# Performance work log

Measured on AMD Instinct MI355X. Metric: run time of the kernel, lower is better.

Reference implementation:

```python
import jax, jax.numpy as jnp
import numpy as np

# |V| = 1,048,576 -> depth = bit_length(|V|-1) = 20, perfect binary tree
DEPTH = 20
N_DIMS = 128
SIZE = (1 << (DEPTH + 1)) - 1  # 2,097,151 tree nodes, each a Linear(n_dims,1) weight row


def setup_inputs() -> dict:
    key = jax.random.key(0)
    # all nn.Linear(n_dims, 1, bias=False) weights stacked into one [SIZE, N_DIMS] table
    W = jax.random.normal(key, (SIZE, N_DIMS), dtype=jnp.float32) * 0.02
    return {"W": W, "v_j_idx": 12345, "u_k_idx": 777777}


def _root_to_leaf_path(u_k_idx):
    # tree index of the leaf is u_k + 2^depth - 1; path node at level l of the
    # perfect tree is ((leaf_idx + 1) >> (depth - l)) - 1, for l = 0..depth.
    t = jnp.asarray(u_k_idx, dtype=jnp.int32) + (1 << DEPTH)  # tgt_idx + 1
    levels = jnp.arange(DEPTH + 1, dtype=jnp.int32)
    return jnp.right_shift(t, DEPTH - levels) - 1  # [depth+1], root -> leaf


def reference(W, v_j_idx, u_k_idx):
    leaf_off = (1 << DEPTH) - 1
    # x = nodes[v_leaf].weight.clone().data  (detached copy of the leaf's weight row)
    x = jax.lax.stop_gradient(W[v_j_idx + leaf_off])  # [n_dims]
    path = _root_to_leaf_path(u_k_idx)                # [depth+1]
    logits = W[path] @ x                              # [depth+1] tiny gather + dot
    prob_of_collocation = jnp.prod(jax.nn.sigmoid(logits))
    return prob_of_collocation.reshape(1, 1)          # matches torch [1,1] output
```

## Files before the change

### kernel.cpp

```cpp
#include <hip/hip_runtime.h>
#include <hip/hip_bf16.h>

#define BT_DEPTH 20
#define BT_NDIMS 128

__global__ __launch_bounds__(256) void BinaryTree_18734647345500_kernel(
    const float* __restrict__ W,
    const int* __restrict__ v_j_idx,
    const int* __restrict__ u_k_idx,
    float* __restrict__ out)
{
    __shared__ float xs[BT_NDIMS];
    __shared__ float logits[BT_DEPTH + 1];

    const int tid  = threadIdx.x;
    const int wave = tid >> 6;
    const int lane = tid & 63;

    const int v = v_j_idx[0];
    const int u = u_k_idx[0];

    const long long leaf = (long long)v + ((1 << BT_DEPTH) - 1);
    if (tid < BT_NDIMS) {
        xs[tid] = W[leaf * BT_NDIMS + tid];
    }
    __syncthreads();

    const unsigned t = (unsigned)u + (1u << BT_DEPTH);

    for (int l = wave; l <= BT_DEPTH; l += 4) {
        const long long node = (long long)(t >> (BT_DEPTH - l)) - 1;
        const float* __restrict__ row = W + node * (long long)BT_NDIMS;

        const float2 rv = *(const float2*)(row + lane * 2);
        const float2 xv = *(const float2*)(&xs[lane * 2]);
        float s = rv.x * xv.x + rv.y * xv.y;

        s += __shfl_xor(s, 32, 64);
        s += __shfl_xor(s, 16, 64);
        s += __shfl_xor(s,  8, 64);
        s += __shfl_xor(s,  4, 64);
        s += __shfl_xor(s,  2, 64);
        s += __shfl_xor(s,  1, 64);

        if (lane == 0) logits[l] = s;
    }
    __syncthreads();

    if (tid == 0) {
        float p = 1.0f;
        #pragma unroll
        for (int l = 0; l <= BT_DEPTH; ++l) {
            const float z = logits[l];
            p *= 1.0f / (1.0f + expf(-z));
        }
        out[0] = p;
    }
}

extern "C" void kernel_launch(void* const* d_in, const int* in_sizes, int n_in,
                              void* d_out, int out_size, void* d_ws, size_t ws_size,
                              hipStream_t stream) {
    const float* W   = (const float*)d_in[0];
    const int*   vj  = (const int*)d_in[1];
    const int*   uk  = (const int*)d_in[2];
    float*       out = (float*)d_out;

    hipLaunchKernelGGL(BinaryTree_18734647345500_kernel,
                       dim3(1), dim3(256), 0, stream,
                       W, vj, uk, out);
}
```

Baseline: 11.61 us.

## Issue all path-row loads up front and fold sigmoid products per wave

Each wave now loads its copy of the leaf row straight into registers, so the shared-memory staging and the first barrier are gone. All six path-row loads per wave are issued together in an unrolled loop, so their latencies overlap instead of running one after another. Each wave's lane 0 computes the sigmoid product for its own levels, and thread 0 only multiplies four partial products. In exchange, waves 1-3 issue one redundant load, which is clamped to the leaf row, and more registers are used.

```diff
diff --git a/kernel.cpp b/kernel.cpp
--- a/kernel.cpp
+++ b/kernel.cpp
@@ -10,8 +10,7 @@
     const int* __restrict__ u_k_idx,
     float* __restrict__ out)
 {
-    __shared__ float xs[BT_NDIMS];
-    __shared__ float logits[BT_DEPTH + 1];
+    __shared__ float pp[4];
 
     const int tid  = threadIdx.x;
     const int wave = tid >> 6;
@@ -21,40 +20,45 @@
     const int u = u_k_idx[0];
 
     const long long leaf = (long long)v + ((1 << BT_DEPTH) - 1);
-    if (tid < BT_NDIMS) {
-        xs[tid] = W[leaf * BT_NDIMS + tid];
+    const unsigned  t    = (unsigned)u + (1u << BT_DEPTH);
+
+    const float2 xv = *(const float2*)(W + leaf * BT_NDIMS + lane * 2);
+
+    float z[6];
+    #pragma unroll
+    for (int i = 0; i < 6; ++i) {
+        const int l = wave + 4 * i;
+        const int shift = (l <= BT_DEPTH) ? (BT_DEPTH - l) : 0;
+        const long long node = (long long)(t >> shift) - 1;
+        const float2 rv = *(const float2*)(W + node * (long long)BT_NDIMS + lane * 2);
+        z[i] = rv.x * xv.x + rv.y * xv.y;
     }
-    __syncthreads();
 
-    const unsigned t = (unsigned)u + (1u << BT_DEPTH);
-
-    for (int l = wave; l <= BT_DEPTH; l += 4) {
-        const long long node = (long long)(t >> (BT_DEPTH - l)) - 1;
-        const float* __restrict__ row = W + node * (long long)BT_NDIMS;
-
-        const float2 rv = *(const float2*)(row + lane * 2);
-        const float2 xv = *(const float2*)(&xs[lane * 2]);
-        float s = rv.x * xv.x + rv.y * xv.y;
-
+    #pragma unroll
+    for (int i = 0; i < 6; ++i) {
+        float s = z[i];
         s += __shfl_xor(s, 32, 64);
         s += __shfl_xor(s, 16, 64);
         s += __shfl_xor(s,  8, 64);
         s += __shfl_xor(s,  4, 64);
         s += __shfl_xor(s,  2, 64);
         s += __shfl_xor(s,  1, 64);
+        z[i] = s;
+    }
 
-        if (lane == 0) logits[l] = s;
+    if (lane == 0) {
+        const int nlev = (wave == 0) ? 6 : 5;
+        float p = 1.0f;
+        #pragma unroll
+        for (int i = 0; i < 6; ++i) {
+            if (i < nlev) p *= 1.0f / (1.0f + expf(-z[i]));
+        }
+        pp[wave] = p;
     }
     __syncthreads();
 
     if (tid == 0) {
-        float p = 1.0f;
-        #pragma unroll
-        for (int l = 0; l <= BT_DEPTH; ++l) {
-            const float z = logits[l];
-            p *= 1.0f / (1.0f + expf(-z));
-        }
-        out[0] = p;
+        out[0] = pp[0] * pp[1] * pp[2] * pp[3];
     }
 }
 
```

After: 9.339 us. 19.5% less time.

## Collapse binary-tree path dot products into a single wave with DPP reductions

Applied to the files above, without the earlier changes.

Replaces the 4-wave block that staged x in LDS and synchronised twice with a single 64-lane wave. Each 16-lane group computes one path node's dot product over 8 elements per lane, reduces with DPP row-shift adds, and accumulates products of (1+exp(-z)). A final reciprocal is taken after readlane combination, which removes shared memory, barriers and per-level divisions. Each lane now issues more loads serially and relies on fast __expf, which may slightly change numerics.

```diff
diff --git a/kernel.cpp b/kernel.cpp
--- a/kernel.cpp
+++ b/kernel.cpp
@@ -4,57 +4,60 @@
 #define BT_DEPTH 20
 #define BT_NDIMS 128
 
-__global__ __launch_bounds__(256) void BinaryTree_18734647345500_kernel(
+template <int CTRL>
+__device__ __forceinline__ float dpp_row_shr_add(float v) {
+    int sh = __builtin_amdgcn_update_dpp(0, __float_as_int(v), CTRL, 0xF, 0xF, true);
+    return v + __int_as_float(sh);
+}
+
+__global__ __launch_bounds__(64) void BinaryTree_18734647345500_kernel(
     const float* __restrict__ W,
     const int* __restrict__ v_j_idx,
     const int* __restrict__ u_k_idx,
     float* __restrict__ out)
 {
-    __shared__ float xs[BT_NDIMS];
-    __shared__ float logits[BT_DEPTH + 1];
-
-    const int tid  = threadIdx.x;
-    const int wave = tid >> 6;
-    const int lane = tid & 63;
+    const int lane = threadIdx.x;
+    const int g    = lane >> 4;
+    const int d    = lane & 15;
 
     const int v = v_j_idx[0];
     const int u = u_k_idx[0];
 
     const long long leaf = (long long)v + ((1 << BT_DEPTH) - 1);
-    if (tid < BT_NDIMS) {
-        xs[tid] = W[leaf * BT_NDIMS + tid];
+    const unsigned  t    = (unsigned)u + (1u << BT_DEPTH);
+
+    const float* xrow = W + leaf * BT_NDIMS + d * 8;
+    const float4 x0 = *(const float4*)(xrow);
+    const float4 x1 = *(const float4*)(xrow + 4);
+
+    float qp = 1.0f;
+
+    #pragma unroll
+    for (int i = 0; i < 6; ++i) {
+        const int l = i * 4 + g;
+        if (l <= BT_DEPTH) {
+            const long long node = (long long)(t >> (BT_DEPTH - l)) - 1;
+            const float* row = W + node * (long long)BT_NDIMS + d * 8;
+            const float4 r0 = *(const float4*)(row);
+            const float4 r1 = *(const float4*)(row + 4);
+            float s = r0.x * x0.x + r0.y * x0.y + r0.z * x0.z + r0.w * x0.w
+                    + r1.x * x1.x + r1.y * x1.y + r1.z * x1.z + r1.w * x1.w;
+            s = dpp_row_shr_add<0x111>(s);
+            s = dpp_row_shr_add<0x112>(s);
+            s = dpp_row_shr_add<0x114>(s);
+            s = dpp_row_shr_add<0x118>(s);
+            const float q = 1.0f + __expf(-s);
+            if (d == 15) qp *= q;
+        }
     }
-    __syncthreads();
 
-    const unsigned t = (unsigned)u + (1u << BT_DEPTH);
+    const float r15 = __uint_as_float(__builtin_amdgcn_readlane(__float_as_uint(qp), 15));
+    const float r31 = __uint_as_float(__builtin_amdgcn_readlane(__float_as_uint(qp), 31));
+    const float r47 = __uint_as_float(__builtin_amdgcn_readlane(__float_as_uint(qp), 47));
+    const float r63 = __uint_as_float(__builtin_amdgcn_readlane(__float_as_uint(qp), 63));
 
-    for (int l = wave; l <= BT_DEPTH; l += 4) {
-        const long long node = (long long)(t >> (BT_DEPTH - l)) - 1;
-        const float* __restrict__ row = W + node * (long long)BT_NDIMS;
-
-        const float2 rv = *(const float2*)(row + lane * 2);
-        const float2 xv = *(const float2*)(&xs[lane * 2]);
-        float s = rv.x * xv.x + rv.y * xv.y;
-
-        s += __shfl_xor(s, 32, 64);
-        s += __shfl_xor(s, 16, 64);
-        s += __shfl_xor(s,  8, 64);
-        s += __shfl_xor(s,  4, 64);
-        s += __shfl_xor(s,  2, 64);
-        s += __shfl_xor(s,  1, 64);
-
-        if (lane == 0) logits[l] = s;
-    }
-    __syncthreads();
-
-    if (tid == 0) {
-        float p = 1.0f;
-        #pragma unroll
-        for (int l = 0; l <= BT_DEPTH; ++l) {
-            const float z = logits[l];
-            p *= 1.0f / (1.0f + expf(-z));
-        }
-        out[0] = p;
+    if (lane == 0) {
+        out[0] = 1.0f / (r15 * r31 * r47 * r63);
     }
 }
 
@@ -67,6 +70,6 @@
     float*       out = (float*)d_out;
 
     hipLaunchKernelGGL(BinaryTree_18734647345500_kernel,
-                       dim3(1), dim3(256), 0, stream,
+                       dim3(1), dim3(64), 0, stream,
                        W, vj, uk, out);
 }
```

Measured after the change: 10.93 us. 5.8% less time.
